# Optimization experiments

Hardware: AMD Instinct MI355X
Metric: run time of the kernel (lower is better)

The kernel has to match this reference:

```python
import jax, jax.numpy as jnp
import numpy as np

D_MODEL = 1024
NUM_HEADS = 16
HEAD_DIM = D_MODEL // NUM_HEADS


def setup_inputs() -> dict:
    key = jax.random.key(0)
    ks = jax.random.split(key, 11)
    B, S, D = 2, 2048, D_MODEL
    scale = 1.0 / np.sqrt(D)
    inp = {
        "query": jax.random.normal(ks[0], (B, S, D), jnp.float32),
        "key": jax.random.normal(ks[1], (B, S, D), jnp.float32),
        "value": jax.random.normal(ks[2], (B, S, D), jnp.float32),
        "Wq": jax.random.normal(ks[3], (D, D), jnp.float32) * scale,
        "bq": jnp.zeros((D,), jnp.float32),
        "Wk": jax.random.normal(ks[4], (D, D), jnp.float32) * scale,
        "bk": jnp.zeros((D,), jnp.float32),
        "Wv": jax.random.normal(ks[5], (D, D), jnp.float32) * scale,
        "bv": jnp.zeros((D,), jnp.float32),
        "Wo": jax.random.normal(ks[6], (D, D), jnp.float32) * scale,
        "bo": jnp.zeros((D,), jnp.float32),
    }
    return inp


def reference(query, key, value, Wq, bq, Wk, bk, Wv, bv, Wo, bo):
    B, S, D = query.shape
    H, hd = NUM_HEADS, HEAD_DIM
    # linear projections (x @ W^T + b, torch nn.Linear convention)
    Q = query @ Wq.T + bq
    K = key @ Wk.T + bk
    V = value @ Wv.T + bv
    # split heads: [B, S, H, hd] -> [B, H, S, hd]
    Q = Q.reshape(B, S, H, hd).transpose(0, 2, 1, 3)
    K = K.reshape(B, S, H, hd).transpose(0, 2, 1, 3)
    V = V.reshape(B, S, H, hd).transpose(0, 2, 1, 3)
    # scaled dot-product attention (explicit, non-flash)
    scores = jnp.einsum("bhqd,bhkd->bhqk", Q, K) / jnp.sqrt(jnp.float32(hd)).astype(Q.dtype)
    attn = jax.nn.softmax(scores, axis=-1)
    out = jnp.einsum("bhqk,bhkd->bhqd", attn, V)
    # merge heads: [B, H, S, hd] -> [B, S, D]
    out = out.transpose(0, 2, 1, 3).reshape(B, S, D)
    return out @ Wo.T + bo
```

## Files before the change

### kernel.cpp

```cpp
#include <hip/hip_runtime.h>
#include <hip/hip_bf16.h>


constexpr int D_MODEL = 1024;
constexpr int S_LEN   = 2048;
constexpr int BATCH   = 2;
constexpr int NH      = 16;
constexpr int HD      = 64;
constexpr int ROWS    = BATCH * S_LEN;

typedef __attribute__((ext_vector_type(8))) short short8;
typedef __attribute__((ext_vector_type(4))) float float4a;

static __device__ __forceinline__ unsigned short f2bf(float f) {
  union { float f; unsigned u; } v{f};
  unsigned r = v.u + 0x7FFFu + ((v.u >> 16) & 1u);
  return (unsigned short)(r >> 16);
}

static __device__ __forceinline__ unsigned pack_bf16(float a, float b) {
#if __has_builtin(__builtin_amdgcn_cvt_pk_bf16_f32)
  typedef __attribute__((ext_vector_type(2))) __bf16 bf16x2;
  union { bf16x2 v; unsigned u; } c;
  c.v = __builtin_amdgcn_cvt_pk_bf16_f32(a, b);
  return c.u;
#else
  return (unsigned)f2bf(a) | ((unsigned)f2bf(b) << 16);
#endif
}

static __device__ __forceinline__ float bf2f(unsigned short u) {
  union { unsigned u; float f; } v;
  v.u = (unsigned)u << 16;
  return v.f;
}

static __device__ __forceinline__ void async16(const void* g, void* l) {
  __builtin_amdgcn_global_load_lds(
      (const __attribute__((address_space(1))) unsigned int*)g,
      (__attribute__((address_space(3))) unsigned int*)l, 16, 0, 0);
}

#define WAIT_LGKM0_SB() do { \
  asm volatile("s_waitcnt lgkmcnt(0)" ::: "memory"); \
  __builtin_amdgcn_sched_barrier(0); } while (0)
#define WAIT_VM0_SB() do { \
  asm volatile("s_waitcnt vmcnt(0)" ::: "memory"); \
  __builtin_amdgcn_sched_barrier(0); } while (0)
#define BARRIER_SB() do { \
  __builtin_amdgcn_s_barrier(); \
  __builtin_amdgcn_sched_barrier(0); } while (0)

struct ConvArgs { const float* s[4]; unsigned short* d[4]; int n[4]; };

__global__ __launch_bounds__(256) void convert_bf16(ConvArgs a) {
  const int which = blockIdx.y;
  const int i = (blockIdx.x * 256 + threadIdx.x) * 8;
  if (i >= a.n[which]) return;
  const float4* s = (const float4*)(a.s[which] + i);
  float4 x = s[0], y = s[1];
  unsigned t[4] = {pack_bf16(x.x, x.y), pack_bf16(x.z, x.w),
                   pack_bf16(y.x, y.y), pack_bf16(y.z, y.w)};
  *(short8*)(a.d[which] + i) = *(short8*)t;
}

template <int MODE>
static __device__ __forceinline__ void gemm_body(
    const float* __restrict__ A, const unsigned short* __restrict__ W,
    const float* __restrict__ bias, void* __restrict__ Yv, float scale,
    unsigned short* As, unsigned short* Bsb, unsigned short* Tb) {
  const int tid = threadIdx.x;
  const int w = tid >> 6, lane = tid & 63;
  const int l15 = lane & 15, quad = lane >> 4;
  const int row0 = blockIdx.x * 128, col0 = blockIdx.y * 128;
  const int wm = (w & 1) * 64, wn = (w >> 1) * 64;

  int rA[4], cA[4];
#pragma unroll
  for (int j = 0; j < 4; j++) {
    const int i = w * 4 + j;
    rA[j] = i * 8 + (lane >> 3);
    cA[j] = ((lane & 7) - (rA[j] >> 1)) & 7;
  }

  float4 av[4][2];
  auto loadA = [&](int kt) {
#pragma unroll
    for (int j = 0; j < 4; j++) {
      const float* s = A + (size_t)(row0 + rA[j]) * D_MODEL + kt + cA[j] * 8;
      av[j][0] = *(const float4*)s;
      av[j][1] = *(const float4*)(s + 4);
    }
  };
  auto loadW = [&](int kt, unsigned short* Bdst) {
#pragma unroll
    for (int j = 0; j < 4; j++) {
      const int i = w * 4 + j;
      async16(W + (size_t)(col0 + rA[j]) * D_MODEL + kt + cA[j] * 8,
              (char*)Bdst + i * 1024);
    }
  };

  float4a acc[4][4];
#pragma unroll
  for (int i = 0; i < 4; i++)
#pragma unroll
    for (int j = 0; j < 4; j++) acc[i][j] = (float4a){0.f, 0.f, 0.f, 0.f};

  loadA(0);
  loadW(0, Bsb);

  for (int kt = 0; kt < D_MODEL; kt += 64) {
    const int cur = (kt >> 6) & 1;
    unsigned short* Bc = Bsb + cur * (128 * 64);
    unsigned short* Bn = Bsb + (cur ^ 1) * (128 * 64);
    const bool more = (kt + 64 < D_MODEL);

    WAIT_LGKM0_SB();
    BARRIER_SB();
    WAIT_VM0_SB();
#pragma unroll
    for (int j = 0; j < 4; j++) {
      unsigned t[4] = {pack_bf16(av[j][0].x, av[j][0].y), pack_bf16(av[j][0].z, av[j][0].w),
                       pack_bf16(av[j][1].x, av[j][1].y), pack_bf16(av[j][1].z, av[j][1].w)};
      *(short8*)((char*)As + (w * 4 + j) * 1024 + (size_t)lane * 16) = *(short8*)t;
    }
    if (more) loadA(kt + 64);
    WAIT_LGKM0_SB();
    BARRIER_SB();
    if (more) loadW(kt + 64, Bn);

#pragma unroll
    for (int kk = 0; kk < 2; kk++) {
      const int sw = (kk * 4 + quad + (l15 >> 1)) & 7;
      short8 af[4], bf[4];
#pragma unroll
      for (int mt = 0; mt < 4; mt++) {
        const int r = wm + mt * 16 + l15;
        af[mt] = *(const short8*)&As[(r * 8 + sw) * 8];
      }
#pragma unroll
      for (int nt = 0; nt < 4; nt++) {
        const int r = wn + nt * 16 + l15;
        bf[nt] = *(const short8*)&Bc[(r * 8 + sw) * 8];
      }
#pragma unroll
      for (int mt = 0; mt < 4; mt++)
#pragma unroll
        for (int nt = 0; nt < 4; nt++)
          acc[mt][nt] = __builtin_amdgcn_mfma_f32_16x16x32_bf16(af[mt], bf[nt], acc[mt][nt], 0, 0, 0);
    }
  }

  int cols[4];
  float bvs[4];
#pragma unroll
  for (int nt = 0; nt < 4; nt++) {
    cols[nt] = col0 + wn + nt * 16 + l15;
    bvs[nt]  = bias[cols[nt]] * ((MODE == 0) ? scale : 1.0f);
  }

  if constexpr (MODE == 0) {
    unsigned short* Y = (unsigned short*)Yv;
#pragma unroll
    for (int mt = 0; mt < 4; mt++)
#pragma unroll
      for (int r = 0; r < 4; r++) {
        const int m = row0 + wm + mt * 16 + quad * 4 + r;
        const int bb = m >> 11, s = m & 2047;
#pragma unroll
        for (int nt = 0; nt < 4; nt++) {
          const int h = cols[nt] >> 6, d = cols[nt] & 63;
          Y[(((size_t)(bb * NH + h)) * S_LEN + s) * HD + d] =
              f2bf(acc[mt][nt][r] * scale + bvs[nt]);
        }
      }
  } else {
    __syncthreads();
    unsigned short* T = Tb + w * (64 * 32);
    unsigned short* Y = (unsigned short*)Yv;
#pragma unroll
    for (int p = 0; p < 2; p++) {
      if (p) { asm volatile("s_waitcnt lgkmcnt(0)" ::: "memory"); }
#pragma unroll
      for (int mi = 0; mi < 2; mi++) {
        const int mt = 2 * p + mi;
#pragma unroll
        for (int r = 0; r < 4; r++) {
          const int sl = mi * 16 + quad * 4 + r;
          const int cch = sl >> 3;
#pragma unroll
          for (int nt = 0; nt < 4; nt++) {
            const int dl = nt * 16 + l15;
            const int slot = cch ^ (dl & 3);
            T[dl * 32 + slot * 8 + (sl & 7)] = f2bf(acc[mt][nt][r] + bvs[nt]);
          }
        }
      }
      asm volatile("s_waitcnt lgkmcnt(0)" ::: "memory");
#pragma unroll
      for (int j = 0; j < 4; j++) {
        const int cid = j * 64 + lane;
        const int dl = cid >> 2;
        const int c  = cid & 3;
        const int slot = c ^ (dl & 3);
        short8 v = *(const short8*)&T[dl * 32 + slot * 8];
        const int col = col0 + wn + dl;
        const int h = col >> 6, d = col & 63;
        const int m = row0 + wm + p * 32 + c * 8;
        const int bb = m >> 11, s = m & 2047;
        *(short8*)&Y[(((size_t)(bb * NH + h)) * HD + d) * S_LEN + s] = v;
      }
    }
  }
}

__global__ __launch_bounds__(256) void gemm_qkv(
    const float* xq, const float* xk, const float* xv,
    const unsigned short* wq, const unsigned short* wk, const unsigned short* wv,
    const float* bq, const float* bk, const float* bv,
    unsigned short* Q, unsigned short* K, unsigned short* Vt) {
  __shared__ unsigned short smem[3 * 128 * 64];
  unsigned short* As  = smem;
  unsigned short* Bsb = smem + 128 * 64;
  unsigned short* Tb  = smem;
  const int z = blockIdx.z;
  if (z == 0)      gemm_body<0>(xq, wq, bq, Q,  0.125f * 1.44269504f, As, Bsb, Tb);
  else if (z == 1) gemm_body<0>(xk, wk, bk, K,  1.0f, As, Bsb, Tb);
  else             gemm_body<2>(xv, wv, bv, Vt, 1.0f, As, Bsb, Tb);
}

__global__ __launch_bounds__(256) void gemm_o(
    const unsigned short* __restrict__ Op, const float* __restrict__ Lp,
    const unsigned short* __restrict__ wo, const float* __restrict__ bo,
    float* __restrict__ out) {
  __shared__ unsigned short As[64 * 64];
  __shared__ unsigned short Bsb[2 * 128 * 64];
  const int tid = threadIdx.x;
  const int w = tid >> 6, lane = tid & 63;
  const int l15 = lane & 15, quad = lane >> 4;
  const int row0 = blockIdx.x * 64, col0 = blockIdx.y * 128;
  const int wn = w * 32;

  const int ar = w * 16 + (lane >> 2);
  const int cg = lane & 3;
  const int asl0 = (cg + (ar >> 1)) & 7;
  const int asl1 = (cg + 4 + (ar >> 1)) & 7;
  const int grow = row0 + ar;
  const unsigned short* P0 = Op + (size_t)grow * D_MODEL + cg * 8;
  const unsigned short* P1 = P0 + (size_t)ROWS * D_MODEL;
  const float* L0 = Lp + (size_t)grow * NH;
  const float* L1 = L0 + (size_t)ROWS * NH;

  int rB[4], cB[4];
#pragma unroll
  for (int j = 0; j < 4; j++) {
    const int i = w * 4 + j;
    rB[j] = i * 8 + (lane >> 3);
    cB[j] = ((lane & 7) - (rB[j] >> 1)) & 7;
  }
  auto loadW = [&](int kt, unsigned short* Bdst) {
#pragma unroll
    for (int j = 0; j < 4; j++) {
      const int i = w * 4 + j;
      async16(wo + (size_t)(col0 + rB[j]) * D_MODEL + kt + cB[j] * 8,
              (char*)Bdst + i * 1024);
    }
  };

  float4a acc[4][2];
#pragma unroll
  for (int i = 0; i < 4; i++)
#pragma unroll
    for (int j = 0; j < 2; j++) acc[i][j] = (float4a){0.f, 0.f, 0.f, 0.f};

  short8 a0 = *(const short8*)(P0 + 0);
  short8 a1 = *(const short8*)(P0 + 32);
  short8 b0 = *(const short8*)(P1 + 0);
  short8 b1 = *(const short8*)(P1 + 32);
  float l0r = L0[0], l1r = L1[0];
  loadW(0, Bsb);

  for (int kt = 0; kt < D_MODEL; kt += 64) {
    const int cur = (kt >> 6) & 1;
    unsigned short* Bc = Bsb + cur * (128 * 64);
    unsigned short* Bn = Bsb + (cur ^ 1) * (128 * 64);
    const bool more = (kt + 64 < D_MODEL);

    WAIT_LGKM0_SB();
    BARRIER_SB();
    WAIT_VM0_SB();
    {
      const float rinv = 1.0f / (l0r + l1r);
      unsigned t0[4], t1[4];
#pragma unroll
      for (int i = 0; i < 4; i++) {
        const float u0 = (bf2f((unsigned short)a0[2 * i]) + bf2f((unsigned short)b0[2 * i])) * rinv;
        const float u1 = (bf2f((unsigned short)a0[2 * i + 1]) + bf2f((unsigned short)b0[2 * i + 1])) * rinv;
        t0[i] = pack_bf16(u0, u1);
        const float v0 = (bf2f((unsigned short)a1[2 * i]) + bf2f((unsigned short)b1[2 * i])) * rinv;
        const float v1 = (bf2f((unsigned short)a1[2 * i + 1]) + bf2f((unsigned short)b1[2 * i + 1])) * rinv;
        t1[i] = pack_bf16(v0, v1);
      }
      *(short8*)&As[(ar * 8 + asl0) * 8] = *(short8*)t0;
      *(short8*)&As[(ar * 8 + asl1) * 8] = *(short8*)t1;
    }
    if (more) {
      const int ktn = kt + 64, hn = ktn >> 6;
      a0 = *(const short8*)(P0 + ktn);
      a1 = *(const short8*)(P0 + ktn + 32);
      b0 = *(const short8*)(P1 + ktn);
      b1 = *(const short8*)(P1 + ktn + 32);
      l0r = L0[hn];
      l1r = L1[hn];
    }
    WAIT_LGKM0_SB();
    BARRIER_SB();
    if (more) loadW(kt + 64, Bn);

#pragma unroll
    for (int kk = 0; kk < 2; kk++) {
      const int sw = (kk * 4 + quad + (l15 >> 1)) & 7;
      short8 af[4], bf[2];
#pragma unroll
      for (int mt = 0; mt < 4; mt++) {
        const int r = mt * 16 + l15;
        af[mt] = *(const short8*)&As[(r * 8 + sw) * 8];
      }
#pragma unroll
      for (int nt = 0; nt < 2; nt++) {
        const int r = wn + nt * 16 + l15;
        bf[nt] = *(const short8*)&Bc[(r * 8 + sw) * 8];
      }
#pragma unroll
      for (int mt = 0; mt < 4; mt++)
#pragma unroll
        for (int nt = 0; nt < 2; nt++)
          acc[mt][nt] = __builtin_amdgcn_mfma_f32_16x16x32_bf16(af[mt], bf[nt], acc[mt][nt], 0, 0, 0);
    }
  }

#pragma unroll
  for (int nt = 0; nt < 2; nt++) {
    const int col = col0 + wn + nt * 16 + l15;
    const float bv = bo[col];
#pragma unroll
    for (int mt = 0; mt < 4; mt++)
#pragma unroll
      for (int r = 0; r < 4; r++) {
        const int m = row0 + mt * 16 + quad * 4 + r;
        out[(size_t)m * D_MODEL + col] = acc[mt][nt][r] + bv;
      }
  }
}

__global__ __launch_bounds__(256) void attn_kernel(
    const unsigned short* __restrict__ Qh, const unsigned short* __restrict__ Kh,
    const unsigned short* __restrict__ Vt, unsigned short* __restrict__ Op,
    float* __restrict__ Lp) {
  const int n   = blockIdx.x;
  const int idx = n >> 3;
  const int qb  = idx & 15;
  const int g   = (n & 7) + 8 * (idx >> 4);
  const int h   = g & 15;
  const int z   = g >> 4;
  const int bb  = z >> 1, sp = z & 1;

  const int tid = threadIdx.x;
  const int w = tid >> 6, lane = tid & 63;
  const int l15 = lane & 15, quad = lane >> 4;

  __shared__ unsigned short Ks[64 * 64];
  __shared__ unsigned short Vs[64 * 64];
  __shared__ unsigned short Ps[4][32][72];

  const size_t bh = (size_t)(bb * NH + h);
  const unsigned short* Qp = Qh + bh * S_LEN * HD;
  const unsigned short* Kp = Kh + bh * S_LEN * HD;
  const unsigned short* Vp = Vt + bh * (size_t)HD * S_LEN;

  const int r0 = w * 16 + (lane >> 3);
  const int c0 = ((lane & 7) - r0) & 7;
  const unsigned short* Kg0 = Kp + (size_t)r0 * HD + c0 * 8;
  const unsigned short* Kg1 = Kg0 + 8 * HD;
  const unsigned short* Vg0 = Vp + (size_t)r0 * S_LEN + c0 * 8;
  const unsigned short* Vg1 = Vg0 + 8 * S_LEN;
  unsigned short* Kd0 = (unsigned short*)((char*)Ks + (w * 2) * 1024 + (size_t)lane * 16);
  unsigned short* Kd1 = (unsigned short*)((char*)Kd0 + 1024);
  unsigned short* Vd0 = (unsigned short*)((char*)Vs + (w * 2) * 1024 + (size_t)lane * 16);
  unsigned short* Vd1 = (unsigned short*)((char*)Vd0 + 1024);

  short8 qf[2][2];
#pragma unroll
  for (int qnt = 0; qnt < 2; qnt++)
#pragma unroll
    for (int c = 0; c < 2; c++)
      qf[qnt][c] = *(const short8*)(Qp + (size_t)(qb * 128 + w * 32 + qnt * 16 + l15) * HD +
                                    c * 32 + quad * 8);

  unsigned short ob[8] = {0x3F80, 0x3F80, 0x3F80, 0x3F80, 0x3F80, 0x3F80, 0x3F80, 0x3F80};
  const short8 ones = *(short8*)ob;

  float4a Oacc[2][4];
#pragma unroll
  for (int a = 0; a < 2; a++)
#pragma unroll
    for (int b = 0; b < 4; b++) Oacc[a][b] = (float4a){0.f, 0.f, 0.f, 0.f};
  float4a Lacc[2] = {(float4a){0.f, 0.f, 0.f, 0.f}, (float4a){0.f, 0.f, 0.f, 0.f}};

  const int sw0 = (quad + l15) & 7;
  const int sw1 = (quad + 4 + l15) & 7;

  const int kb0 = sp * 1024, kbend = kb0 + 1024;

  short8 kr0 = *(const short8*)(Kg0 + (size_t)kb0 * HD);
  short8 kr1 = *(const short8*)(Kg1 + (size_t)kb0 * HD);
  short8 vr0 = *(const short8*)(Vg0 + kb0);
  short8 vr1 = *(const short8*)(Vg1 + kb0);

  for (int kb = kb0; kb < kbend; kb += 64) {
    asm volatile("s_waitcnt lgkmcnt(0)" ::: "memory");
    __builtin_amdgcn_sched_barrier(0);
    __builtin_amdgcn_s_barrier();
    asm volatile("s_waitcnt vmcnt(0)" ::: "memory");
    __builtin_amdgcn_sched_barrier(0);
    *(short8*)Kd0 = kr0;
    *(short8*)Kd1 = kr1;
    *(short8*)Vd0 = vr0;
    *(short8*)Vd1 = vr1;
    if (kb + 64 < kbend) {
      kr0 = *(const short8*)(Kg0 + (size_t)(kb + 64) * HD);
      kr1 = *(const short8*)(Kg1 + (size_t)(kb + 64) * HD);
      vr0 = *(const short8*)(Vg0 + (kb + 64));
      vr1 = *(const short8*)(Vg1 + (kb + 64));
    }
    asm volatile("s_waitcnt lgkmcnt(0)" ::: "memory");
    __builtin_amdgcn_sched_barrier(0);
    __builtin_amdgcn_s_barrier();

#pragma unroll
    for (int mt = 0; mt < 4; mt++) {
      const int rb = (mt * 16 + l15) * 8;
      short8 a0 = *(const short8*)&Ks[(rb + sw0) * 8];
      short8 a1 = *(const short8*)&Ks[(rb + sw1) * 8];
#pragma unroll
      for (int qnt = 0; qnt < 2; qnt++) {
        float4a s = (float4a){0.f, 0.f, 0.f, 0.f};
        s = __builtin_amdgcn_mfma_f32_16x16x32_bf16(a0, qf[qnt][0], s, 0, 0, 0);
        s = __builtin_amdgcn_mfma_f32_16x16x32_bf16(a1, qf[qnt][1], s, 0, 0, 0);
        uint2 pk;
        pk.x = pack_bf16(__builtin_amdgcn_exp2f(s[0]), __builtin_amdgcn_exp2f(s[1]));
        pk.y = pack_bf16(__builtin_amdgcn_exp2f(s[2]), __builtin_amdgcn_exp2f(s[3]));
        *(uint2*)&Ps[w][qnt * 16 + l15][mt * 16 + quad * 4] = pk;
      }
    }
    asm volatile("s_waitcnt lgkmcnt(0)" ::: "memory");

#pragma unroll
    for (int c = 0; c < 2; c++) {
      short8 pa0 = *(const short8*)&Ps[w][l15][c * 32 + quad * 8];
      short8 pa1 = *(const short8*)&Ps[w][16 + l15][c * 32 + quad * 8];
      Lacc[0] = __builtin_amdgcn_mfma_f32_16x16x32_bf16(pa0, ones, Lacc[0], 0, 0, 0);
      Lacc[1] = __builtin_amdgcn_mfma_f32_16x16x32_bf16(pa1, ones, Lacc[1], 0, 0, 0);
      const int vsw = (c * 4 + quad + l15) & 7;
#pragma unroll
      for (int nt = 0; nt < 4; nt++) {
        short8 vb = *(const short8*)&Vs[((nt * 16 + l15) * 8 + vsw) * 8];
        Oacc[0][nt] = __builtin_amdgcn_mfma_f32_16x16x32_bf16(pa0, vb, Oacc[0][nt], 0, 0, 0);
        Oacc[1][nt] = __builtin_amdgcn_mfma_f32_16x16x32_bf16(pa1, vb, Oacc[1][nt], 0, 0, 0);
      }
    }
  }

  if (l15 == 0) {
#pragma unroll
    for (int qnt = 0; qnt < 2; qnt++)
#pragma unroll
      for (int reg = 0; reg < 4; reg++) {
        const int q = qb * 128 + w * 32 + qnt * 16 + quad * 4 + reg;
        Lp[(size_t)sp * ROWS * NH + ((size_t)bb * S_LEN + q) * NH + h] = Lacc[qnt][reg];
      }
  }

  unsigned short* Ob = Op + (size_t)sp * ROWS * D_MODEL;
#pragma unroll
  for (int qnt = 0; qnt < 2; qnt++) {
#pragma unroll
    for (int reg = 0; reg < 4; reg++) {
      const int q = qb * 128 + w * 32 + qnt * 16 + quad * 4 + reg;
      unsigned short* orow = Ob + ((size_t)bb * S_LEN + q) * D_MODEL + h * HD;
#pragma unroll
      for (int nt = 0; nt < 4; nt++)
        orow[nt * 16 + l15] = f2bf(Oacc[qnt][nt][reg]);
    }
  }
}

extern "C" void kernel_launch(void* const* d_in, const int* in_sizes, int n_in,
                              void* d_out, int out_size, void* d_ws, size_t ws_size,
                              hipStream_t stream) {
  const float* query = (const float*)d_in[0];
  const float* key   = (const float*)d_in[1];
  const float* value = (const float*)d_in[2];
  const float* Wq = (const float*)d_in[3];
  const float* bq = (const float*)d_in[4];
  const float* Wk = (const float*)d_in[5];
  const float* bk = (const float*)d_in[6];
  const float* Wv = (const float*)d_in[7];
  const float* bv = (const float*)d_in[8];
  const float* Wo = (const float*)d_in[9];
  const float* bo = (const float*)d_in[10];
  float* out = (float*)d_out;

  char* ws = (char*)d_ws;
  const size_t MB = 1024 * 1024;
  unsigned short* wq16 = (unsigned short*)(ws + 24 * MB);
  unsigned short* wk16 = (unsigned short*)(ws + 26 * MB);
  unsigned short* wv16 = (unsigned short*)(ws + 28 * MB);
  unsigned short* qbuf  = (unsigned short*)(ws + 32 * MB);
  unsigned short* kbuf  = (unsigned short*)(ws + 40 * MB);
  unsigned short* vtbuf = (unsigned short*)(ws + 48 * MB);
  unsigned short* wo16  = (unsigned short*)(ws + 56 * MB);
  float* Lp = (float*)(ws + 58 * MB);
  unsigned short* Op = (unsigned short*)(ws + 0 * MB);

  ConvArgs ca;
  const int NW = D_MODEL * D_MODEL;
  ca.s[0] = Wq; ca.d[0] = wq16; ca.n[0] = NW;
  ca.s[1] = Wk; ca.d[1] = wk16; ca.n[1] = NW;
  ca.s[2] = Wv; ca.d[2] = wv16; ca.n[2] = NW;
  ca.s[3] = Wo; ca.d[3] = wo16; ca.n[3] = NW;
  hipLaunchKernelGGL(convert_bf16, dim3(NW / 2048, 4), dim3(256), 0, stream, ca);

  dim3 gqkv(ROWS / 128, D_MODEL / 128, 3);
  hipLaunchKernelGGL(gemm_qkv, gqkv, dim3(256), 0, stream,
                     query, key, value, wq16, wk16, wv16, bq, bk, bv,
                     qbuf, kbuf, vtbuf);

  hipLaunchKernelGGL(attn_kernel, dim3(1024), dim3(256), 0, stream,
                     qbuf, kbuf, vtbuf, Op, Lp);

  dim3 go(ROWS / 64, D_MODEL / 128);
  hipLaunchKernelGGL(gemm_o, go, dim3(256), 0, stream, Op, Lp, wo16, bo, out);
}
```

Before: 232.0 us.

## Shrink QKV GEMM tile to 64x128 and load weights through registers

```diff
diff --git a/kernel.cpp b/kernel.cpp
--- a/kernel.cpp
+++ b/kernel.cpp
@@ -68,94 +68,97 @@
 static __device__ __forceinline__ void gemm_body(
     const float* __restrict__ A, const unsigned short* __restrict__ W,
     const float* __restrict__ bias, void* __restrict__ Yv, float scale,
-    unsigned short* As, unsigned short* Bsb, unsigned short* Tb) {
+    int row0, int col0,
+    unsigned short* As, unsigned short* Bs, unsigned short* Tb) {
   const int tid = threadIdx.x;
   const int w = tid >> 6, lane = tid & 63;
   const int l15 = lane & 15, quad = lane >> 4;
-  const int row0 = blockIdx.x * 128, col0 = blockIdx.y * 128;
-  const int wm = (w & 1) * 64, wn = (w >> 1) * 64;
-
-  int rA[4], cA[4];
-#pragma unroll
-  for (int j = 0; j < 4; j++) {
-    const int i = w * 4 + j;
-    rA[j] = i * 8 + (lane >> 3);
-    cA[j] = ((lane & 7) - (rA[j] >> 1)) & 7;
-  }
-
-  float4 av[4][2];
+  const int wn = w * 32;
+
+  const int ar = w * 16 + (lane >> 2);
+  const int cg = lane & 3;
+  const int asl0 = (cg + (ar >> 1)) & 7;
+  const int asl1 = (cg + 4 + (ar >> 1)) & 7;
+  const float* Ag = A + (size_t)(row0 + ar) * D_MODEL + cg * 8;
+
+  const int wr = w * 32 + (lane >> 1);
+  const int wc = lane & 1;
+  int wsl[4];
+#pragma unroll
+  for (int j = 0; j < 4; j++) wsl[j] = (wc * 4 + j + (wr >> 1)) & 7;
+  const unsigned short* Wg = W + (size_t)(col0 + wr) * D_MODEL + wc * 32;
+
+  float4 av[4];
+  short8 wv[4];
   auto loadA = [&](int kt) {
-#pragma unroll
-    for (int j = 0; j < 4; j++) {
-      const float* s = A + (size_t)(row0 + rA[j]) * D_MODEL + kt + cA[j] * 8;
-      av[j][0] = *(const float4*)s;
-      av[j][1] = *(const float4*)(s + 4);
-    }
+    const float* s = Ag + kt;
+    av[0] = *(const float4*)s;
+    av[1] = *(const float4*)(s + 4);
+    av[2] = *(const float4*)(s + 32);
+    av[3] = *(const float4*)(s + 36);
   };
-  auto loadW = [&](int kt, unsigned short* Bdst) {
-#pragma unroll
-    for (int j = 0; j < 4; j++) {
-      const int i = w * 4 + j;
-      async16(W + (size_t)(col0 + rA[j]) * D_MODEL + kt + cA[j] * 8,
-              (char*)Bdst + i * 1024);
-    }
+  auto loadW = [&](int kt) {
+    const unsigned short* s = Wg + kt;
+#pragma unroll
+    for (int j = 0; j < 4; j++) wv[j] = *(const short8*)(s + j * 8);
   };
 
-  float4a acc[4][4];
+  float4a acc[4][2];
 #pragma unroll
   for (int i = 0; i < 4; i++)
 #pragma unroll
-    for (int j = 0; j < 4; j++) acc[i][j] = (float4a){0.f, 0.f, 0.f, 0.f};
+    for (int j = 0; j < 2; j++) acc[i][j] = (float4a){0.f, 0.f, 0.f, 0.f};
 
   loadA(0);
-  loadW(0, Bsb);
+  loadW(0);
 
   for (int kt = 0; kt < D_MODEL; kt += 64) {
-    const int cur = (kt >> 6) & 1;
-    unsigned short* Bc = Bsb + cur * (128 * 64);
-    unsigned short* Bn = Bsb + (cur ^ 1) * (128 * 64);
     const bool more = (kt + 64 < D_MODEL);
 
     WAIT_LGKM0_SB();
     BARRIER_SB();
     WAIT_VM0_SB();
-#pragma unroll
-    for (int j = 0; j < 4; j++) {
-      unsigned t[4] = {pack_bf16(av[j][0].x, av[j][0].y), pack_bf16(av[j][0].z, av[j][0].w),
-                       pack_bf16(av[j][1].x, av[j][1].y), pack_bf16(av[j][1].z, av[j][1].w)};
-      *(short8*)((char*)As + (w * 4 + j) * 1024 + (size_t)lane * 16) = *(short8*)t;
-    }
-    if (more) loadA(kt + 64);
+    {
+      unsigned t0[4] = {pack_bf16(av[0].x, av[0].y), pack_bf16(av[0].z, av[0].w),
+                        pack_bf16(av[1].x, av[1].y), pack_bf16(av[1].z, av[1].w)};
+      unsigned t1[4] = {pack_bf16(av[2].x, av[2].y), pack_bf16(av[2].z, av[2].w),
+                        pack_bf16(av[3].x, av[3].y), pack_bf16(av[3].z, av[3].w)};
+      *(short8*)&As[(ar * 8 + asl0) * 8] = *(short8*)t0;
+      *(short8*)&As[(ar * 8 + asl1) * 8] = *(short8*)t1;
+#pragma unroll
+      for (int j = 0; j < 4; j++)
+        *(short8*)&Bs[(wr * 8 + wsl[j]) * 8] = wv[j];
+    }
+    if (more) { loadA(kt + 64); loadW(kt + 64); }
     WAIT_LGKM0_SB();
     BARRIER_SB();
-    if (more) loadW(kt + 64, Bn);
 
 #pragma unroll
     for (int kk = 0; kk < 2; kk++) {
       const int sw = (kk * 4 + quad + (l15 >> 1)) & 7;
-      short8 af[4], bf[4];
+      short8 af[4], bf[2];
 #pragma unroll
       for (int mt = 0; mt < 4; mt++) {
-        const int r = wm + mt * 16 + l15;
+        const int r = mt * 16 + l15;
         af[mt] = *(const short8*)&As[(r * 8 + sw) * 8];
       }
 #pragma unroll
-      for (int nt = 0; nt < 4; nt++) {
+      for (int nt = 0; nt < 2; nt++) {
         const int r = wn + nt * 16 + l15;
-        bf[nt] = *(const short8*)&Bc[(r * 8 + sw) * 8];
+        bf[nt] = *(const short8*)&Bs[(r * 8 + sw) * 8];
       }
 #pragma unroll
       for (int mt = 0; mt < 4; mt++)
 #pragma unroll
-        for (int nt = 0; nt < 4; nt++)
+        for (int nt = 0; nt < 2; nt++)
           acc[mt][nt] = __builtin_amdgcn_mfma_f32_16x16x32_bf16(af[mt], bf[nt], acc[mt][nt], 0, 0, 0);
     }
   }
 
-  int cols[4];
-  float bvs[4];
-#pragma unroll
-  for (int nt = 0; nt < 4; nt++) {
+  int cols[2];
+  float bvs[2];
+#pragma unroll
+  for (int nt = 0; nt < 2; nt++) {
     cols[nt] = col0 + wn + nt * 16 + l15;
     bvs[nt]  = bias[cols[nt]] * ((MODE == 0) ? scale : 1.0f);
   }
@@ -166,10 +169,10 @@
     for (int mt = 0; mt < 4; mt++)
 #pragma unroll
       for (int r = 0; r < 4; r++) {
-        const int m = row0 + wm + mt * 16 + quad * 4 + r;
+        const int m = row0 + mt * 16 + quad * 4 + r;
         const int bb = m >> 11, s = m & 2047;
 #pragma unroll
-        for (int nt = 0; nt < 4; nt++) {
+        for (int nt = 0; nt < 2; nt++) {
           const int h = cols[nt] >> 6, d = cols[nt] & 63;
           Y[(((size_t)(bb * NH + h)) * S_LEN + s) * HD + d] =
               f2bf(acc[mt][nt][r] * scale + bvs[nt]);
@@ -177,7 +180,7 @@
       }
   } else {
     __syncthreads();
-    unsigned short* T = Tb + w * (64 * 32);
+    unsigned short* T = Tb + w * (32 * 32);
     unsigned short* Y = (unsigned short*)Yv;
 #pragma unroll
     for (int p = 0; p < 2; p++) {
@@ -190,7 +193,7 @@
           const int sl = mi * 16 + quad * 4 + r;
           const int cch = sl >> 3;
 #pragma unroll
-          for (int nt = 0; nt < 4; nt++) {
+          for (int nt = 0; nt < 2; nt++) {
             const int dl = nt * 16 + l15;
             const int slot = cch ^ (dl & 3);
             T[dl * 32 + slot * 8 + (sl & 7)] = f2bf(acc[mt][nt][r] + bvs[nt]);
@@ -199,7 +202,7 @@
       }
       asm volatile("s_waitcnt lgkmcnt(0)" ::: "memory");
 #pragma unroll
-      for (int j = 0; j < 4; j++) {
+      for (int j = 0; j < 2; j++) {
         const int cid = j * 64 + lane;
         const int dl = cid >> 2;
         const int c  = cid & 3;
@@ -207,7 +210,7 @@
         short8 v = *(const short8*)&T[dl * 32 + slot * 8];
         const int col = col0 + wn + dl;
         const int h = col >> 6, d = col & 63;
-        const int m = row0 + wm + p * 32 + c * 8;
+        const int m = row0 + p * 32 + c * 8;
         const int bb = m >> 11, s = m & 2047;
         *(short8*)&Y[(((size_t)(bb * NH + h)) * HD + d) * S_LEN + s] = v;
       }
@@ -220,14 +223,15 @@
     const unsigned short* wq, const unsigned short* wk, const unsigned short* wv,
     const float* bq, const float* bk, const float* bv,
     unsigned short* Q, unsigned short* K, unsigned short* Vt) {
-  __shared__ unsigned short smem[3 * 128 * 64];
-  unsigned short* As  = smem;
-  unsigned short* Bsb = smem + 128 * 64;
-  unsigned short* Tb  = smem;
+  __shared__ unsigned short smem[64 * 64 + 128 * 64];
+  unsigned short* As = smem;
+  unsigned short* Bs = smem + 64 * 64;
+  unsigned short* Tb = smem;
   const int z = blockIdx.z;
-  if (z == 0)      gemm_body<0>(xq, wq, bq, Q,  0.125f * 1.44269504f, As, Bsb, Tb);
-  else if (z == 1) gemm_body<0>(xk, wk, bk, K,  1.0f, As, Bsb, Tb);
-  else             gemm_body<2>(xv, wv, bv, Vt, 1.0f, As, Bsb, Tb);
+  const int row0 = blockIdx.x * 64, col0 = blockIdx.y * 128;
+  if (z == 0)      gemm_body<0>(xq, wq, bq, Q,  0.125f * 1.44269504f, row0, col0, As, Bs, Tb);
+  else if (z == 1) gemm_body<0>(xk, wk, bk, K,  1.0f, row0, col0, As, Bs, Tb);
+  else             gemm_body<2>(xv, wv, bv, Vt, 1.0f, row0, col0, As, Bs, Tb);
 }
 
 __global__ __launch_bounds__(256) void gemm_o(
@@ -532,7 +536,7 @@
   ca.s[3] = Wo; ca.d[3] = wo16; ca.n[3] = NW;
   hipLaunchKernelGGL(convert_bf16, dim3(NW / 2048, 4), dim3(256), 0, stream, ca);
 
-  dim3 gqkv(ROWS / 128, D_MODEL / 128, 3);
+  dim3 gqkv(ROWS / 64, D_MODEL / 128, 3);
   hipLaunchKernelGGL(gemm_qkv, gqkv, dim3(256), 0, stream,
                      query, key, value, wq16, wk16, wv16, bq, bk, bv,
                      qbuf, kbuf, vtbuf);
```

Result: slower. 237.7 us (+2.5%).
